# Kernel tuning notes

Hardware: AMD Instinct MI355X
Metric: run time of the kernel (lower is better)

Reference implementation:

```python
import jax, jax.numpy as jnp
import numpy as np

EMBED_DIM = 1024
NUM_HEADS = 16
HEAD_DIM = EMBED_DIM // NUM_HEADS


def setup_inputs() -> dict:
    key = jax.random.key(0)
    ks = jax.random.split(key, 6)
    B, S, D = 4, 2048, EMBED_DIM
    std = 1.0 / np.sqrt(D)
    x = jax.random.normal(ks[0], (B, S, D), dtype=jnp.float32)
    wq = jax.random.normal(ks[1], (D, D), dtype=jnp.float32) * std
    wk = jax.random.normal(ks[2], (D, D), dtype=jnp.float32) * std
    wv = jax.random.normal(ks[3], (D, D), dtype=jnp.float32) * std
    wo = jax.random.normal(ks[4], (D, D), dtype=jnp.float32) * std
    bo = jax.random.normal(ks[5], (D,), dtype=jnp.float32) * 0.01
    return {"x": x, "wq": wq, "wk": wk, "wv": wv, "wo": wo, "bo": bo}


def reference(x, wq, wk, wv, wo, bo):
    B, S, D = x.shape
    H, Hd = NUM_HEADS, HEAD_DIM
    scale = 1.0 / jnp.sqrt(jnp.asarray(Hd, x.dtype))
    # nn.Linear computes x @ W.T; split into heads -> [B, H, S, Hd]
    q = (x @ wq.T).reshape(B, S, H, Hd).transpose(0, 2, 1, 3)
    k = (x @ wk.T).reshape(B, S, H, Hd).transpose(0, 2, 1, 3)
    v = (x @ wv.T).reshape(B, S, H, Hd).transpose(0, 2, 1, 3)
    scores = jnp.einsum("bhqd,bhkd->bhqk", q, k) * scale  # [B,H,S,S]
    attn = jax.nn.softmax(scores, axis=-1)
    ctx = jnp.einsum("bhqk,bhkd->bhqd", attn, v)
    ctx = ctx.transpose(0, 2, 1, 3).reshape(B, S, D)
    return ctx @ wo.T + bo
```

## Files before the change

### kernel.cpp

```cpp
#include <hip/hip_runtime.h>

typedef __bf16 bf16x8 __attribute__((ext_vector_type(8)));
typedef float f32x4 __attribute__((ext_vector_type(4)));
typedef unsigned u32x4 __attribute__((ext_vector_type(4)));
typedef unsigned short u16;

#define GAS __attribute__((address_space(1)))
#define LAS __attribute__((address_space(3)))

static __device__ __forceinline__ void gload16(const void* g, void* l) {
  __builtin_amdgcn_global_load_lds((const GAS unsigned int*)g, (LAS unsigned int*)l, 16, 0, 0);
}

static __device__ __forceinline__ u16 f2bf(float f) {
  unsigned u = __builtin_bit_cast(unsigned, f);
  u += 0x7fffu + ((u >> 16) & 1u);
  return (u16)(u >> 16);
}

static __device__ __forceinline__ unsigned pk2(float lo, float hi) {
  ushort2 u;
  u.x = __builtin_bit_cast(u16, (__bf16)lo);
  u.y = __builtin_bit_cast(u16, (__bf16)hi);
  return __builtin_bit_cast(unsigned, u);
}

static __device__ __forceinline__ f32x4 vmax4(f32x4 a, f32x4 b) {
  f32x4 r;
  r[0] = fmaxf(a[0], b[0]); r[1] = fmaxf(a[1], b[1]);
  r[2] = fmaxf(a[2], b[2]); r[3] = fmaxf(a[3], b[3]);
  return r;
}

__global__ void cvt_kernel(const float* __restrict__ src, u16* __restrict__ dst, int n4) {
  int i = blockIdx.x * 256 + threadIdx.x;
  if (i >= n4) return;
  float4 v = reinterpret_cast<const float4*>(src)[i];
  ushort4 o;
  o.x = f2bf(v.x); o.y = f2bf(v.y); o.z = f2bf(v.z); o.w = f2bf(v.w);
  reinterpret_cast<ushort4*>(dst)[i] = o;
}

__global__ void cvt_w_kernel(const float* __restrict__ w0, const float* __restrict__ w1,
                             const float* __restrict__ w2, const float* __restrict__ w3,
                             u16* __restrict__ d0, u16* __restrict__ d1,
                             u16* __restrict__ d2, u16* __restrict__ d3) {
  int sel = blockIdx.x >> 10;
  int i = (blockIdx.x & 1023) * 256 + threadIdx.x;
  const float* s = sel == 0 ? w0 : sel == 1 ? w1 : sel == 2 ? w2 : w3;
  u16* d = sel == 0 ? d0 : sel == 1 ? d1 : sel == 2 ? d2 : d3;
  float4 v = reinterpret_cast<const float4*>(s)[i];
  ushort4 o;
  o.x = f2bf(v.x); o.y = f2bf(v.y); o.z = f2bf(v.z); o.w = f2bf(v.w);
  reinterpret_cast<ushort4*>(d)[i] = o;
}

__global__ void gemm_qkv(const u16* __restrict__ A, const u16* __restrict__ W,
                         u16* __restrict__ Qo, u16* __restrict__ Ko, u16* __restrict__ Vo) {
  __shared__ u16 As[128 * 32];
  __shared__ u16 Bs[128 * 32];
  const int t = threadIdx.x;
  const int lane = t & 63;
  const int w = t >> 6;
  const int wr = w >> 1, wc = w & 1;
  const int l15 = lane & 15, lhi = lane >> 4;
  const int swz = (blockIdx.x & 7) * 192 + (blockIdx.x >> 3);
  const int bm = swz / 24, bn = swz % 24;

  f32x4 acc[4][4];
#pragma unroll
  for (int a = 0; a < 4; ++a)
#pragma unroll
    for (int b = 0; b < 4; ++b) acc[a][b] = (f32x4){0.f, 0.f, 0.f, 0.f};

  const u16* ag = A + (size_t)(bm * 128 + (t >> 2)) * 1024 + (t & 3) * 8;
  const u16* bg = W + (size_t)(bn * 128 + (t >> 2)) * 1024 + (t & 3) * 8;
  u16* as_p = &As[t * 8];
  u16* bs_p = &Bs[t * 8];

  for (int kt = 0; kt < 32; ++kt) {
    gload16(ag, as_p);
    gload16(ag + 64 * 1024, as_p + 2048);
    gload16(bg, bs_p);
    gload16(bg + 64 * 1024, bs_p + 2048);
    ag += 32; bg += 32;
    __syncthreads();
    bf16x8 af[4], bfr[4];
#pragma unroll
    for (int mt = 0; mt < 4; ++mt)
      af[mt] = *(const bf16x8*)&As[(wr * 64 + mt * 16 + l15) * 32 + lhi * 8];
#pragma unroll
    for (int nt = 0; nt < 4; ++nt)
      bfr[nt] = *(const bf16x8*)&Bs[(wc * 64 + nt * 16 + l15) * 32 + lhi * 8];
#pragma unroll
    for (int mt = 0; mt < 4; ++mt)
#pragma unroll
      for (int nt = 0; nt < 4; ++nt)
        acc[mt][nt] = __builtin_amdgcn_mfma_f32_16x16x32_bf16(af[mt], bfr[nt], acc[mt][nt], 0, 0, 0);
    __syncthreads();
  }

  const int tsel = bn >> 3;
  const int m0 = bm * 128 + wr * 64;
  const int n0 = bn * 128 + wc * 64;
  const int bb = bm >> 4;
  if (tsel == 0) {
    const float qs = 0.125f * 1.4426950408889634f;
#pragma unroll
    for (int nt = 0; nt < 4; ++nt) {
      int n = n0 + nt * 16 + l15;
      int c = n & 1023, h = c >> 6, hd = c & 63;
      size_t base = (size_t)(bb * 16 + h) * 2048 * 64 + hd;
#pragma unroll
      for (int mt = 0; mt < 4; ++mt)
#pragma unroll
        for (int i = 0; i < 4; ++i) {
          int s = (m0 + mt * 16 + lhi * 4 + i) & 2047;
          Qo[base + (size_t)s * 64] = f2bf(acc[mt][nt][i] * qs);
        }
    }
  } else if (tsel == 1) {
#pragma unroll
    for (int nt = 0; nt < 4; ++nt) {
      int n = n0 + nt * 16 + l15;
      int c = n & 1023, h = c >> 6, hd = c & 63;
      size_t base = (size_t)(bb * 16 + h) * 2048 * 64 + hd;
#pragma unroll
      for (int mt = 0; mt < 4; ++mt)
#pragma unroll
        for (int i = 0; i < 4; ++i) {
          int s = (m0 + mt * 16 + lhi * 4 + i) & 2047;
          Ko[base + (size_t)s * 64] = f2bf(acc[mt][nt][i]);
        }
    }
  } else {
#pragma unroll
    for (int nt = 0; nt < 4; ++nt) {
      int n = n0 + nt * 16 + l15;
      int c = n & 1023, h = c >> 6, hd = c & 63;
#pragma unroll
      for (int mt = 0; mt < 4; ++mt) {
        int s0 = (m0 + mt * 16 + lhi * 4) & 2047;
        int sp0 = ((s0 >> 4) & 1) * 4 + ((s0 >> 2) & 3) * 8 + (s0 >> 5) * 32;
        ushort4 pk;
        pk.x = f2bf(acc[mt][nt][0]);
        pk.y = f2bf(acc[mt][nt][1]);
        pk.z = f2bf(acc[mt][nt][2]);
        pk.w = f2bf(acc[mt][nt][3]);
        *(ushort4*)&Vo[((size_t)(bb * 16 + h) * 64 + hd) * 2048 + sp0] = pk;
      }
    }
  }
}

__global__ __launch_bounds__(512, 4) void attn_kernel(const u16* __restrict__ Q,
                                                      const u16* __restrict__ K,
                                                      const u16* __restrict__ Vp,
                                                      u16* __restrict__ Ctx) {
  __shared__ u16 Ks[2 * 128 * 64];
  __shared__ u16 Vs[2 * 64 * 128];
  const int t = threadIdx.x;
  const int lane = t & 63;
  const int w = t >> 6;
  const int l15 = lane & 15, lhi = lane >> 4;
  const int swz = (blockIdx.x & 7) * 64 + (blockIdx.x >> 3);
  const int pair = swz >> 3, qt = swz & 7;
  const u16* qp = Q + (size_t)pair * 2048 * 64;
  const u16* kp = K + (size_t)pair * 2048 * 64;
  const u16* vp = Vp + (size_t)pair * 64 * 2048;

  const int qrA = qt * 256 + w * 32 + l15;
  bf16x8 qfA[2], qfB[2];
  qfA[0] = *(const bf16x8*)&qp[(size_t)qrA * 64 + lhi * 8];
  qfA[1] = *(const bf16x8*)&qp[(size_t)qrA * 64 + 32 + lhi * 8];
  qfB[0] = *(const bf16x8*)&qp[(size_t)(qrA + 16) * 64 + lhi * 8];
  qfB[1] = *(const bf16x8*)&qp[(size_t)(qrA + 16) * 64 + 32 + lhi * 8];

  const int swzq = (l15 & 7) << 3;
  const int kofs0 = l15 * 64 + ((lhi * 8) ^ swzq);
  const int kofs1 = l15 * 64 + ((32 + lhi * 8) ^ swzq);
  const int vofs0 = l15 * 128 + ((lhi * 8) ^ swzq);
  const int vofs1 = l15 * 128 + ((32 + lhi * 8) ^ swzq);

  float mA = -1e30f, lA = 0.f, mB = -1e30f, lB = 0.f;
  f32x4 coA[4], coB[4];
#pragma unroll
  for (int n = 0; n < 4; ++n) { coA[n] = (f32x4){0.f, 0.f, 0.f, 0.f}; coB[n] = coA[n]; }

  auto stage = [&](int cb, int tt) {
#pragma unroll
    for (int j = 0; j < 2; ++j) {
      int c = j * 512 + t;
      int r = c >> 3, c8 = (c & 7) * 8;
      gload16(kp + (size_t)(tt * 128 + r) * 64 + (c8 ^ ((r & 7) << 3)), &Ks[cb + c * 8]);
    }
#pragma unroll
    for (int j = 0; j < 2; ++j) {
      int c = j * 512 + t;
      int r = c >> 4, c8 = (c & 15) * 8;
      gload16(vp + (size_t)r * 2048 + tt * 128 + (c8 ^ ((r & 7) << 3)), &Vs[cb + c * 8]);
    }
  };

  auto softmax_step = [&](f32x4 (&sa)[8], float& m, float& l, f32x4 (&co)[4],
                          unsigned (&pw)[8][2]) {
    f32x4 t0 = vmax4(vmax4(sa[0], sa[1]), vmax4(sa[2], sa[3]));
    f32x4 t2 = vmax4(vmax4(sa[4], sa[5]), vmax4(sa[6], sa[7]));
    t0 = vmax4(t0, t2);
    float mx = fmaxf(fmaxf(t0[0], t0[1]), fmaxf(t0[2], t0[3]));
    mx = fmaxf(mx, __shfl_xor(mx, 16));
    mx = fmaxf(mx, __shfl_xor(mx, 32));
    float mn = m;
    if (!__all(mx - m <= 8.0f)) {
      mn = fmaxf(m, mx);
      float sc = __builtin_exp2f(m - mn);
      l *= sc;
      float si0 = __shfl(sc, lhi * 4 + 0);
      float si1 = __shfl(sc, lhi * 4 + 1);
      float si2 = __shfl(sc, lhi * 4 + 2);
      float si3 = __shfl(sc, lhi * 4 + 3);
#pragma unroll
      for (int nthd = 0; nthd < 4; ++nthd) {
        co[nthd][0] *= si0; co[nthd][1] *= si1;
        co[nthd][2] *= si2; co[nthd][3] *= si3;
      }
      m = mn;
    }
#pragma unroll
    for (int nt = 0; nt < 8; ++nt)
#pragma unroll
      for (int e = 0; e < 4; ++e) sa[nt][e] = __builtin_exp2f(sa[nt][e] - mn);
    f32x4 s0 = (sa[0] + sa[1]) + (sa[2] + sa[3]);
    f32x4 s2 = (sa[4] + sa[5]) + (sa[6] + sa[7]);
    s0 = s0 + s2;
    float rs = (s0[0] + s0[1]) + (s0[2] + s0[3]);
    rs += __shfl_xor(rs, 16);
    rs += __shfl_xor(rs, 32);
    l += rs;
#pragma unroll
    for (int nt = 0; nt < 8; ++nt) {
      pw[nt][0] = pk2(sa[nt][0], sa[nt][1]);
      pw[nt][1] = pk2(sa[nt][2], sa[nt][3]);
    }
  };

  stage(0, 0);
  __syncthreads();

  for (int kt = 0; kt < 16; ++kt) {
    const int cb = (kt & 1) * 8192;
    if (kt < 15) stage(cb ^ 8192, kt + 1);

    f32x4 saA[8], saB[8];
    __builtin_amdgcn_s_setprio(1);
#pragma unroll
    for (int nt = 0; nt < 8; ++nt) {
      saA[nt] = (f32x4){0.f, 0.f, 0.f, 0.f};
      saB[nt] = saA[nt];
      bf16x8 kf0 = *(const bf16x8*)&Ks[cb + kofs0 + nt * 1024];
      bf16x8 kf1 = *(const bf16x8*)&Ks[cb + kofs1 + nt * 1024];
      saA[nt] = __builtin_amdgcn_mfma_f32_16x16x32_bf16(kf0, qfA[0], saA[nt], 0, 0, 0);
      saB[nt] = __builtin_amdgcn_mfma_f32_16x16x32_bf16(kf0, qfB[0], saB[nt], 0, 0, 0);
      saA[nt] = __builtin_amdgcn_mfma_f32_16x16x32_bf16(kf1, qfA[1], saA[nt], 0, 0, 0);
      saB[nt] = __builtin_amdgcn_mfma_f32_16x16x32_bf16(kf1, qfB[1], saB[nt], 0, 0, 0);
    }
    __builtin_amdgcn_s_setprio(0);

    unsigned pwA[8][2], pwB[8][2];
    softmax_step(saA, mA, lA, coA, pwA);
    softmax_step(saB, mB, lB, coB, pwB);

    __builtin_amdgcn_s_setprio(1);
#pragma unroll
    for (int ks = 0; ks < 4; ++ks) {
      u32x4 awA = {pwA[2 * ks][0], pwA[2 * ks][1], pwA[2 * ks + 1][0], pwA[2 * ks + 1][1]};
      u32x4 awB = {pwB[2 * ks][0], pwB[2 * ks][1], pwB[2 * ks + 1][0], pwB[2 * ks + 1][1]};
      bf16x8 afA = __builtin_bit_cast(bf16x8, awA);
      bf16x8 afB = __builtin_bit_cast(bf16x8, awB);
      const int vo = (ks & 1) ? vofs1 : vofs0;
      const int vhi = (ks >> 1) * 64;
#pragma unroll
      for (int nthd = 0; nthd < 4; ++nthd) {
        bf16x8 vf = *(const bf16x8*)&Vs[cb + vo + vhi + nthd * 2048];
        coA[nthd] = __builtin_amdgcn_mfma_f32_16x16x32_bf16(afA, vf, coA[nthd], 0, 0, 0);
        coB[nthd] = __builtin_amdgcn_mfma_f32_16x16x32_bf16(afB, vf, coB[nthd], 0, 0, 0);
      }
    }
    __builtin_amdgcn_s_setprio(0);
    __syncthreads();
  }

  float liA[4], liB[4];
#pragma unroll
  for (int i = 0; i < 4; ++i) {
    liA[i] = 1.0f / __shfl(lA, lhi * 4 + i);
    liB[i] = 1.0f / __shfl(lB, lhi * 4 + i);
  }
  const int bb = pair >> 4, h = pair & 15;
  const int sbase = qt * 256 + w * 32 + lhi * 4;
#pragma unroll
  for (int nthd = 0; nthd < 4; ++nthd) {
    int hd = nthd * 16 + l15;
#pragma unroll
    for (int i = 0; i < 4; ++i) {
      Ctx[(size_t)(bb * 2048 + sbase + i) * 1024 + h * 64 + hd] = f2bf(coA[nthd][i] * liA[i]);
      Ctx[(size_t)(bb * 2048 + sbase + 16 + i) * 1024 + h * 64 + hd] = f2bf(coB[nthd][i] * liB[i]);
    }
  }
}

__global__ void gemm_out(const u16* __restrict__ A, const u16* __restrict__ W,
                         const float* __restrict__ Bo, float* __restrict__ Out) {
  __shared__ u16 As[128 * 32];
  __shared__ u16 Bs[128 * 32];
  const int t = threadIdx.x;
  const int lane = t & 63;
  const int w = t >> 6;
  const int wr = w >> 1, wc = w & 1;
  const int l15 = lane & 15, lhi = lane >> 4;
  const int swz = (blockIdx.x & 7) * 64 + (blockIdx.x >> 3);
  const int bm = swz >> 3, bn = swz & 7;

  f32x4 acc[4][4];
#pragma unroll
  for (int a = 0; a < 4; ++a)
#pragma unroll
    for (int b = 0; b < 4; ++b) acc[a][b] = (f32x4){0.f, 0.f, 0.f, 0.f};

  const u16* ag = A + (size_t)(bm * 128 + (t >> 2)) * 1024 + (t & 3) * 8;
  const u16* bg = W + (size_t)(bn * 128 + (t >> 2)) * 1024 + (t & 3) * 8;
  u16* as_p = &As[t * 8];
  u16* bs_p = &Bs[t * 8];

  for (int kt = 0; kt < 32; ++kt) {
    gload16(ag, as_p);
    gload16(ag + 64 * 1024, as_p + 2048);
    gload16(bg, bs_p);
    gload16(bg + 64 * 1024, bs_p + 2048);
    ag += 32; bg += 32;
    __syncthreads();
    bf16x8 af[4], bfr[4];
#pragma unroll
    for (int mt = 0; mt < 4; ++mt)
      af[mt] = *(const bf16x8*)&As[(wr * 64 + mt * 16 + l15) * 32 + lhi * 8];
#pragma unroll
    for (int nt = 0; nt < 4; ++nt)
      bfr[nt] = *(const bf16x8*)&Bs[(wc * 64 + nt * 16 + l15) * 32 + lhi * 8];
#pragma unroll
    for (int mt = 0; mt < 4; ++mt)
#pragma unroll
      for (int nt = 0; nt < 4; ++nt)
        acc[mt][nt] = __builtin_amdgcn_mfma_f32_16x16x32_bf16(af[mt], bfr[nt], acc[mt][nt], 0, 0, 0);
    __syncthreads();
  }

  const int m0 = bm * 128 + wr * 64;
  const int n0 = bn * 128 + wc * 64;
#pragma unroll
  for (int nt = 0; nt < 4; ++nt) {
    int n = n0 + nt * 16 + l15;
    float bias = Bo[n];
#pragma unroll
    for (int mt = 0; mt < 4; ++mt)
#pragma unroll
      for (int i = 0; i < 4; ++i) {
        int m = m0 + mt * 16 + lhi * 4 + i;
        Out[(size_t)m * 1024 + n] = acc[mt][nt][i] + bias;
      }
  }
}

extern "C" void kernel_launch(void* const* d_in, const int* in_sizes, int n_in,
                              void* d_out, int out_size, void* d_ws, size_t ws_size,
                              hipStream_t stream) {
  const float* x  = (const float*)d_in[0];
  const float* wq = (const float*)d_in[1];
  const float* wk = (const float*)d_in[2];
  const float* wv = (const float*)d_in[3];
  const float* wo = (const float*)d_in[4];
  const float* bo = (const float*)d_in[5];
  float* out = (float*)d_out;

  u16* xb    = (u16*)d_ws;
  u16* wqkvb = xb + (size_t)8 * 1024 * 1024;
  u16* wob   = wqkvb + (size_t)3 * 1024 * 1024;
  u16* qb    = wob + (size_t)1 * 1024 * 1024;
  u16* kb    = qb + (size_t)8 * 1024 * 1024;
  u16* vtb   = kb + (size_t)8 * 1024 * 1024;
  u16* ctxb  = xb;

  cvt_kernel<<<8192, 256, 0, stream>>>(x, xb, 2097152);
  cvt_w_kernel<<<4096, 256, 0, stream>>>(wq, wk, wv, wo,
                                         wqkvb, wqkvb + 1048576, wqkvb + 2097152, wob);
  gemm_qkv<<<64 * 24, 256, 0, stream>>>(xb, wqkvb, qb, kb, vtb);
  attn_kernel<<<512, 512, 0, stream>>>(qb, kb, vtb, ctxb);
  gemm_out<<<64 * 8, 256, 0, stream>>>(ctxb, wob, bo, out);
}
```

Before: 261.1 us.

## Halve attention block size, split KV tile softmax, compute row sums via MFMA

The attention kernel now runs 1024 blocks of 256 threads, each owning 128 query rows instead of 256. This doubles the K/V tile loads per query row across the grid. Each 128-key tile is processed as two 64-key halves, with a separate online-softmax rescale per half, which shortens the register live range of the score arrays. Row sums are no longer built with VALU adds and cross-lane shuffles; they accumulate through an extra MFMA against a ones vector, which sums the bf16-rounded probabilities and adds MFMA work.

New measurement: 245.5 us. 1.06x faster.

```diff
diff --git a/kernel.cpp b/kernel.cpp
--- a/kernel.cpp
+++ b/kernel.cpp
@@ -153,7 +153,7 @@
   }
 }
 
-__global__ __launch_bounds__(512, 4) void attn_kernel(const u16* __restrict__ Q,
+__global__ __launch_bounds__(256, 2) void attn_kernel(const u16* __restrict__ Q,
                                                       const u16* __restrict__ K,
                                                       const u16* __restrict__ Vp,
                                                       u16* __restrict__ Ctx) {
@@ -163,62 +163,64 @@
   const int lane = t & 63;
   const int w = t >> 6;
   const int l15 = lane & 15, lhi = lane >> 4;
-  const int swz = (blockIdx.x & 7) * 64 + (blockIdx.x >> 3);
-  const int pair = swz >> 3, qt = swz & 7;
+  const int swz = (blockIdx.x & 7) * 128 + (blockIdx.x >> 3);
+  const int qt = swz & 15, pair = swz >> 4;
   const u16* qp = Q + (size_t)pair * 2048 * 64;
   const u16* kp = K + (size_t)pair * 2048 * 64;
   const u16* vp = Vp + (size_t)pair * 64 * 2048;
 
-  const int qrA = qt * 256 + w * 32 + l15;
+  const int qrA = qt * 128 + w * 32 + l15;
   bf16x8 qfA[2], qfB[2];
   qfA[0] = *(const bf16x8*)&qp[(size_t)qrA * 64 + lhi * 8];
   qfA[1] = *(const bf16x8*)&qp[(size_t)qrA * 64 + 32 + lhi * 8];
   qfB[0] = *(const bf16x8*)&qp[(size_t)(qrA + 16) * 64 + lhi * 8];
   qfB[1] = *(const bf16x8*)&qp[(size_t)(qrA + 16) * 64 + 32 + lhi * 8];
 
+  const u32x4 ow = {0x3F803F80u, 0x3F803F80u, 0x3F803F80u, 0x3F803F80u};
+  const bf16x8 onesf = __builtin_bit_cast(bf16x8, ow);
+
   const int swzq = (l15 & 7) << 3;
   const int kofs0 = l15 * 64 + ((lhi * 8) ^ swzq);
   const int kofs1 = l15 * 64 + ((32 + lhi * 8) ^ swzq);
   const int vofs0 = l15 * 128 + ((lhi * 8) ^ swzq);
   const int vofs1 = l15 * 128 + ((32 + lhi * 8) ^ swzq);
 
-  float mA = -1e30f, lA = 0.f, mB = -1e30f, lB = 0.f;
-  f32x4 coA[4], coB[4];
-#pragma unroll
-  for (int n = 0; n < 4; ++n) { coA[n] = (f32x4){0.f, 0.f, 0.f, 0.f}; coB[n] = coA[n]; }
+  float mA = -1e30f, mB = -1e30f;
+  f32x4 coA[4], coB[4], laA, laB;
+  laA = (f32x4){0.f, 0.f, 0.f, 0.f};
+  laB = laA;
+#pragma unroll
+  for (int n = 0; n < 4; ++n) { coA[n] = laA; coB[n] = laA; }
 
   auto stage = [&](int cb, int tt) {
 #pragma unroll
-    for (int j = 0; j < 2; ++j) {
-      int c = j * 512 + t;
+    for (int j = 0; j < 4; ++j) {
+      int c = j * 256 + t;
       int r = c >> 3, c8 = (c & 7) * 8;
       gload16(kp + (size_t)(tt * 128 + r) * 64 + (c8 ^ ((r & 7) << 3)), &Ks[cb + c * 8]);
     }
 #pragma unroll
-    for (int j = 0; j < 2; ++j) {
-      int c = j * 512 + t;
+    for (int j = 0; j < 4; ++j) {
+      int c = j * 256 + t;
       int r = c >> 4, c8 = (c & 15) * 8;
       gload16(vp + (size_t)r * 2048 + tt * 128 + (c8 ^ ((r & 7) << 3)), &Vs[cb + c * 8]);
     }
   };
 
-  auto softmax_step = [&](f32x4 (&sa)[8], float& m, float& l, f32x4 (&co)[4],
-                          unsigned (&pw)[8][2]) {
+  auto softmax_sub = [&](f32x4 (&sa)[4], float& m, f32x4 (&co)[4], f32x4& lacc,
+                         unsigned (&pw)[4][2]) {
     f32x4 t0 = vmax4(vmax4(sa[0], sa[1]), vmax4(sa[2], sa[3]));
-    f32x4 t2 = vmax4(vmax4(sa[4], sa[5]), vmax4(sa[6], sa[7]));
-    t0 = vmax4(t0, t2);
     float mx = fmaxf(fmaxf(t0[0], t0[1]), fmaxf(t0[2], t0[3]));
     mx = fmaxf(mx, __shfl_xor(mx, 16));
     mx = fmaxf(mx, __shfl_xor(mx, 32));
-    float mn = m;
     if (!__all(mx - m <= 8.0f)) {
-      mn = fmaxf(m, mx);
+      float mn = fmaxf(m, mx);
       float sc = __builtin_exp2f(m - mn);
-      l *= sc;
       float si0 = __shfl(sc, lhi * 4 + 0);
       float si1 = __shfl(sc, lhi * 4 + 1);
       float si2 = __shfl(sc, lhi * 4 + 2);
       float si3 = __shfl(sc, lhi * 4 + 3);
+      lacc[0] *= si0; lacc[1] *= si1; lacc[2] *= si2; lacc[3] *= si3;
 #pragma unroll
       for (int nthd = 0; nthd < 4; ++nthd) {
         co[nthd][0] *= si0; co[nthd][1] *= si1;
@@ -227,18 +229,11 @@
       m = mn;
     }
 #pragma unroll
-    for (int nt = 0; nt < 8; ++nt)
-#pragma unroll
-      for (int e = 0; e < 4; ++e) sa[nt][e] = __builtin_exp2f(sa[nt][e] - mn);
-    f32x4 s0 = (sa[0] + sa[1]) + (sa[2] + sa[3]);
-    f32x4 s2 = (sa[4] + sa[5]) + (sa[6] + sa[7]);
-    s0 = s0 + s2;
-    float rs = (s0[0] + s0[1]) + (s0[2] + s0[3]);
-    rs += __shfl_xor(rs, 16);
-    rs += __shfl_xor(rs, 32);
-    l += rs;
-#pragma unroll
-    for (int nt = 0; nt < 8; ++nt) {
+    for (int nt = 0; nt < 4; ++nt)
+#pragma unroll
+      for (int e = 0; e < 4; ++e) sa[nt][e] = __builtin_exp2f(sa[nt][e] - m);
+#pragma unroll
+    for (int nt = 0; nt < 4; ++nt) {
       pw[nt][0] = pk2(sa[nt][0], sa[nt][1]);
       pw[nt][1] = pk2(sa[nt][2], sa[nt][3]);
     }
@@ -251,60 +246,65 @@
     const int cb = (kt & 1) * 8192;
     if (kt < 15) stage(cb ^ 8192, kt + 1);
 
-    f32x4 saA[8], saB[8];
-    __builtin_amdgcn_s_setprio(1);
-#pragma unroll
-    for (int nt = 0; nt < 8; ++nt) {
-      saA[nt] = (f32x4){0.f, 0.f, 0.f, 0.f};
-      saB[nt] = saA[nt];
-      bf16x8 kf0 = *(const bf16x8*)&Ks[cb + kofs0 + nt * 1024];
-      bf16x8 kf1 = *(const bf16x8*)&Ks[cb + kofs1 + nt * 1024];
-      saA[nt] = __builtin_amdgcn_mfma_f32_16x16x32_bf16(kf0, qfA[0], saA[nt], 0, 0, 0);
-      saB[nt] = __builtin_amdgcn_mfma_f32_16x16x32_bf16(kf0, qfB[0], saB[nt], 0, 0, 0);
-      saA[nt] = __builtin_amdgcn_mfma_f32_16x16x32_bf16(kf1, qfA[1], saA[nt], 0, 0, 0);
-      saB[nt] = __builtin_amdgcn_mfma_f32_16x16x32_bf16(kf1, qfB[1], saB[nt], 0, 0, 0);
-    }
-    __builtin_amdgcn_s_setprio(0);
-
-    unsigned pwA[8][2], pwB[8][2];
-    softmax_step(saA, mA, lA, coA, pwA);
-    softmax_step(saB, mB, lB, coB, pwB);
-
-    __builtin_amdgcn_s_setprio(1);
-#pragma unroll
-    for (int ks = 0; ks < 4; ++ks) {
-      u32x4 awA = {pwA[2 * ks][0], pwA[2 * ks][1], pwA[2 * ks + 1][0], pwA[2 * ks + 1][1]};
-      u32x4 awB = {pwB[2 * ks][0], pwB[2 * ks][1], pwB[2 * ks + 1][0], pwB[2 * ks + 1][1]};
-      bf16x8 afA = __builtin_bit_cast(bf16x8, awA);
-      bf16x8 afB = __builtin_bit_cast(bf16x8, awB);
-      const int vo = (ks & 1) ? vofs1 : vofs0;
-      const int vhi = (ks >> 1) * 64;
-#pragma unroll
-      for (int nthd = 0; nthd < 4; ++nthd) {
-        bf16x8 vf = *(const bf16x8*)&Vs[cb + vo + vhi + nthd * 2048];
-        coA[nthd] = __builtin_amdgcn_mfma_f32_16x16x32_bf16(afA, vf, coA[nthd], 0, 0, 0);
-        coB[nthd] = __builtin_amdgcn_mfma_f32_16x16x32_bf16(afB, vf, coB[nthd], 0, 0, 0);
-      }
-    }
-    __builtin_amdgcn_s_setprio(0);
+#pragma unroll
+    for (int h = 0; h < 2; ++h) {
+      f32x4 saA[4], saB[4];
+      __builtin_amdgcn_s_setprio(1);
+#pragma unroll
+      for (int nt4 = 0; nt4 < 4; ++nt4) {
+        const int nt = h * 4 + nt4;
+        saA[nt4] = (f32x4){0.f, 0.f, 0.f, 0.f};
+        saB[nt4] = saA[nt4];
+        bf16x8 kf0 = *(const bf16x8*)&Ks[cb + kofs0 + nt * 1024];
+        bf16x8 kf1 = *(const bf16x8*)&Ks[cb + kofs1 + nt * 1024];
+        saA[nt4] = __builtin_amdgcn_mfma_f32_16x16x32_bf16(kf0, qfA[0], saA[nt4], 0, 0, 0);
+        saB[nt4] = __builtin_amdgcn_mfma_f32_16x16x32_bf16(kf0, qfB[0], saB[nt4], 0, 0, 0);
+        saA[nt4] = __builtin_amdgcn_mfma_f32_16x16x32_bf16(kf1, qfA[1], saA[nt4], 0, 0, 0);
+        saB[nt4] = __builtin_amdgcn_mfma_f32_16x16x32_bf16(kf1, qfB[1], saB[nt4], 0, 0, 0);
+      }
+      __builtin_amdgcn_s_setprio(0);
+
+      unsigned pwA[4][2], pwB[4][2];
+      softmax_sub(saA, mA, coA, laA, pwA);
+      softmax_sub(saB, mB, coB, laB, pwB);
+
+      __builtin_amdgcn_s_setprio(1);
+#pragma unroll
+      for (int ks = 0; ks < 2; ++ks) {
+        u32x4 awA = {pwA[2 * ks][0], pwA[2 * ks][1], pwA[2 * ks + 1][0], pwA[2 * ks + 1][1]};
+        u32x4 awB = {pwB[2 * ks][0], pwB[2 * ks][1], pwB[2 * ks + 1][0], pwB[2 * ks + 1][1]};
+        bf16x8 afA = __builtin_bit_cast(bf16x8, awA);
+        bf16x8 afB = __builtin_bit_cast(bf16x8, awB);
+        laA = __builtin_amdgcn_mfma_f32_16x16x32_bf16(afA, onesf, laA, 0, 0, 0);
+        laB = __builtin_amdgcn_mfma_f32_16x16x32_bf16(afB, onesf, laB, 0, 0, 0);
+        const int vo = (ks ? vofs1 : vofs0) + h * 64;
+#pragma unroll
+        for (int nthd = 0; nthd < 4; ++nthd) {
+          bf16x8 vf = *(const bf16x8*)&Vs[cb + vo + nthd * 2048];
+          coA[nthd] = __builtin_amdgcn_mfma_f32_16x16x32_bf16(afA, vf, coA[nthd], 0, 0, 0);
+          coB[nthd] = __builtin_amdgcn_mfma_f32_16x16x32_bf16(afB, vf, coB[nthd], 0, 0, 0);
+        }
+      }
+      __builtin_amdgcn_s_setprio(0);
+    }
     __syncthreads();
   }
 
   float liA[4], liB[4];
 #pragma unroll
   for (int i = 0; i < 4; ++i) {
-    liA[i] = 1.0f / __shfl(lA, lhi * 4 + i);
-    liB[i] = 1.0f / __shfl(lB, lhi * 4 + i);
-  }
-  const int bb = pair >> 4, h = pair & 15;
-  const int sbase = qt * 256 + w * 32 + lhi * 4;
+    liA[i] = 1.0f / laA[i];
+    liB[i] = 1.0f / laB[i];
+  }
+  const int bb = pair >> 4, hh = pair & 15;
+  const int sbase = qt * 128 + w * 32 + lhi * 4;
 #pragma unroll
   for (int nthd = 0; nthd < 4; ++nthd) {
     int hd = nthd * 16 + l15;
 #pragma unroll
     for (int i = 0; i < 4; ++i) {
-      Ctx[(size_t)(bb * 2048 + sbase + i) * 1024 + h * 64 + hd] = f2bf(coA[nthd][i] * liA[i]);
-      Ctx[(size_t)(bb * 2048 + sbase + 16 + i) * 1024 + h * 64 + hd] = f2bf(coB[nthd][i] * liB[i]);
+      Ctx[(size_t)(bb * 2048 + sbase + i) * 1024 + hh * 64 + hd] = f2bf(coA[nthd][i] * liA[i]);
+      Ctx[(size_t)(bb * 2048 + sbase + 16 + i) * 1024 + hh * 64 + hd] = f2bf(coB[nthd][i] * liB[i]);
     }
   }
 }
@@ -393,6 +393,6 @@
   cvt_w_kernel<<<4096, 256, 0, stream>>>(wq, wk, wv, wo,
                                          wqkvb, wqkvb + 1048576, wqkvb + 2097152, wob);
   gemm_qkv<<<64 * 24, 256, 0, stream>>>(xb, wqkvb, qb, kb, vtb);
-  attn_kernel<<<512, 512, 0, stream>>>(qb, kb, vtb, ctxb);
+  attn_kernel<<<1024, 256, 0, stream>>>(qb, kb, vtb, ctxb);
   gemm_out<<<64 * 8, 256, 0, stream>>>(ctxb, wob, bo, out);
 }
```
